# Optimization experiments

Hardware: AMD Instinct MI355X
Metric: run time of the kernel (lower is better)

Reference implementation:

```python
import jax, jax.numpy as jnp
import numpy as np

B, IN_DIM, HID, ATT = 16384, 128, 512, 256
TOTAL = IN_DIM + HID + ATT


def setup_inputs() -> dict:
    key = jax.random.key(0)
    ks = jax.random.split(key, 10)
    u = lambda k, shape, lo, hi: jax.random.uniform(k, shape, jnp.float32, lo, hi)
    return {
        "t": jnp.float32(0.0),
        "h_ltc": jax.random.normal(ks[0], (B, HID), jnp.float32),
        "x_t": jax.random.normal(ks[1], (B, IN_DIM), jnp.float32),
        "context": jax.random.normal(ks[2], (B, ATT), jnp.float32),
        "W_gd": u(ks[3], (2 * HID, TOTAL), -0.1, 0.1),
        "b_gd": u(ks[4], (2 * HID,), -0.1, 0.1),
        "W_tau": u(ks[5], (HID, HID), -0.1, 0.1),
        "b_tau": u(ks[6], (HID,), -0.1, 0.1),
        "gleak": u(ks[7], (HID,), 0.001, 1.0),
        "cm": u(ks[8], (HID,), 0.4, 0.6),
    }


def reference(t, h_ltc, x_t, context, W_gd, b_gd, W_tau, b_tau, gleak, cm):
    # combined: [B, IN+HID+ATT]
    combined = jnp.concatenate([x_t, h_ltc, context], axis=1)
    g_d = combined @ W_gd.T + b_gd            # [B, 2*HID]
    gate, dynamics = jnp.split(g_d, 2, axis=1)
    tau = jax.nn.softplus(h_ltc @ W_tau.T + b_tau)  # [B, HID]
    numerator = jax.nn.sigmoid(gate) * jnp.tanh(dynamics) - h_ltc
    denominator = tau + jax.nn.softplus(cm) + jax.nn.softplus(gleak)
    return numerator / (denominator + 1e-6)
```

## Files before the change

kernel.cpp:

```cpp
#include <hip/hip_runtime.h>
#include <hip/hip_bf16.h>
#include <math.h>

#define BROWS 16384
#define IN_DIM 128
#define HID 512
#define ATT 256
#define KTOT 896
#define KC_TOT 112

typedef __bf16 bf16x8 __attribute__((ext_vector_type(8)));
typedef float f32x4 __attribute__((ext_vector_type(4)));

__device__ __forceinline__ float softplus_f(float x) {
    return fmaxf(x, 0.0f) + log1pf(__expf(-fabsf(x)));
}

__global__ void pack_B(const float* __restrict__ W_gd, const float* __restrict__ W_tau,
                       const float* __restrict__ gleak, const float* __restrict__ cm,
                       __hip_bfloat16* __restrict__ B_stage, float* __restrict__ dconst) {
    const int cid = blockIdx.x * 256 + threadIdx.x;
    if (cid < HID) {
        dconst[cid] = softplus_f(cm[cid]) + softplus_f(gleak[cid]) + 1e-6f;
    }
    const int nl = cid % 192;
    const int kc = (cid / 192) % KC_TOT;
    const int jt = cid / (192 * KC_TOT);
    const int jg = nl / 48, type = (nl % 48) / 16, j16 = nl % 16;
    const int j = jt * 64 + jg * 16 + j16;
    const int k0 = kc * 8;

    float v[8];
    if (type == 0) {
        const float* s = W_gd + (size_t)j * KTOT + k0;
        #pragma unroll
        for (int i = 0; i < 8; ++i) v[i] = s[i];
    } else if (type == 1) {
        const float* s = W_gd + (size_t)(HID + j) * KTOT + k0;
        #pragma unroll
        for (int i = 0; i < 8; ++i) v[i] = s[i];
    } else {
        if (k0 >= IN_DIM && k0 < IN_DIM + HID) {
            const float* s = W_tau + (size_t)j * HID + (k0 - IN_DIM);
            #pragma unroll
            for (int i = 0; i < 8; ++i) v[i] = s[i];
        } else {
            #pragma unroll
            for (int i = 0; i < 8; ++i) v[i] = 0.0f;
        }
    }
    union { __hip_bfloat16 hh[8]; uint4 u; } p;
    #pragma unroll
    for (int i = 0; i < 8; ++i) p.hh[i] = __float2bfloat16(v[i]);
    *(uint4*)(B_stage + (size_t)cid * 8) = p.u;
}

__global__ __launch_bounds__(1024, 4) void ltc_gemm(
    const float* __restrict__ x, const float* __restrict__ h_ltc,
    const float* __restrict__ ctx, const __hip_bfloat16* __restrict__ B_stage,
    const float* __restrict__ b_gd, const float* __restrict__ b_tau,
    const float* __restrict__ dconst, float* __restrict__ out) {

    __shared__ __attribute__((aligned(16))) char As[114688];

    const int mt = blockIdx.x;
    const int tid = threadIdx.x;
    const int wave = tid >> 6, lane = tid & 63;
    const int q = lane >> 4, t = lane & 15;

    const int mi = tid >> 4;
    const int kcg = tid & 15;
    #pragma unroll
    for (int s = 0; s < 7; ++s) {
        const int kc = kcg + 16 * s;
        const float* src; int rs, col;
        if (s == 0)      { src = x;     rs = IN_DIM; col = kcg * 8; }
        else if (s < 5)  { src = h_ltc; rs = HID;    col = kcg * 8 + (s - 1) * 128; }
        else             { src = ctx;   rs = ATT;    col = kcg * 8 + (s - 5) * 128; }
        const float* p = src + (size_t)(mt * 64 + mi) * rs + col;
        float4 v0 = *(const float4*)p;
        float4 v1 = *(const float4*)(p + 4);
        union { __hip_bfloat16 hh[8]; uint4 u; } pk;
        pk.hh[0] = __float2bfloat16(v0.x); pk.hh[1] = __float2bfloat16(v0.y);
        pk.hh[2] = __float2bfloat16(v0.z); pk.hh[3] = __float2bfloat16(v0.w);
        pk.hh[4] = __float2bfloat16(v1.x); pk.hh[5] = __float2bfloat16(v1.y);
        pk.hh[6] = __float2bfloat16(v1.z); pk.hh[7] = __float2bfloat16(v1.w);
        *(uint4*)(As + ((kc * 64 + (mi ^ (kc & 31))) << 4)) = pk.u;
    }
    __syncthreads();

    for (int it = 0; it < 2; ++it) {
        const int jglob = it * 256 + wave * 16;
        const int jt = jglob >> 6;
        const int jg = (jglob >> 4) & 3;
        const __hip_bfloat16* bBase = B_stage
            + ((size_t)jt * (KC_TOT * 192) + jg * 48 + t) * 8;

        f32x4 acc[4][3];
        #pragma unroll
        for (int f = 0; f < 4; ++f)
            #pragma unroll
            for (int ty = 0; ty < 3; ++ty) acc[f][ty] = (f32x4)0.0f;

        bf16x8 ab[2][4]; bf16x8 bb[2][3];

        {
            const int kc = q;
            ab[0][0] = *(const bf16x8*)(As + ((kc * 64 + (t ^ kc)) << 4));
            ab[0][1] = *(const bf16x8*)(As + ((kc * 64 + ((16 + t) ^ kc)) << 4));
            ab[0][2] = *(const bf16x8*)(As + ((kc * 64 + ((32 + t) ^ kc)) << 4));
            ab[0][3] = *(const bf16x8*)(As + ((kc * 64 + ((48 + t) ^ kc)) << 4));
            const __hip_bfloat16* bp = bBase + (size_t)kc * 1536;
            bb[0][0] = *(const bf16x8*)(bp);
            bb[0][1] = *(const bf16x8*)(bp + 128);
        }

        #pragma unroll 4
        for (int kst = 0; kst < 28; ++kst) {
            const int cb = kst & 1, nb = cb ^ 1;
            const bool tau_cur = (kst >= 4 && kst < 20);
            if (kst < 27) {
                const int kc = (kst + 1) * 4 + q;
                const int sw = kc & 31;
                ab[nb][0] = *(const bf16x8*)(As + ((kc * 64 + (t ^ sw)) << 4));
                ab[nb][1] = *(const bf16x8*)(As + ((kc * 64 + ((16 + t) ^ sw)) << 4));
                ab[nb][2] = *(const bf16x8*)(As + ((kc * 64 + ((32 + t) ^ sw)) << 4));
                ab[nb][3] = *(const bf16x8*)(As + ((kc * 64 + ((48 + t) ^ sw)) << 4));
                const __hip_bfloat16* bp = bBase + (size_t)kc * 1536;
                bb[nb][0] = *(const bf16x8*)(bp);
                bb[nb][1] = *(const bf16x8*)(bp + 128);
                if (kst + 1 >= 4 && kst + 1 < 20)
                    bb[nb][2] = *(const bf16x8*)(bp + 256);
            }
            acc[0][0] = __builtin_amdgcn_mfma_f32_16x16x32_bf16(ab[cb][0], bb[cb][0], acc[0][0], 0, 0, 0);
            acc[1][0] = __builtin_amdgcn_mfma_f32_16x16x32_bf16(ab[cb][1], bb[cb][0], acc[1][0], 0, 0, 0);
            acc[2][0] = __builtin_amdgcn_mfma_f32_16x16x32_bf16(ab[cb][2], bb[cb][0], acc[2][0], 0, 0, 0);
            acc[3][0] = __builtin_amdgcn_mfma_f32_16x16x32_bf16(ab[cb][3], bb[cb][0], acc[3][0], 0, 0, 0);
            acc[0][1] = __builtin_amdgcn_mfma_f32_16x16x32_bf16(ab[cb][0], bb[cb][1], acc[0][1], 0, 0, 0);
            acc[1][1] = __builtin_amdgcn_mfma_f32_16x16x32_bf16(ab[cb][1], bb[cb][1], acc[1][1], 0, 0, 0);
            acc[2][1] = __builtin_amdgcn_mfma_f32_16x16x32_bf16(ab[cb][2], bb[cb][1], acc[2][1], 0, 0, 0);
            acc[3][1] = __builtin_amdgcn_mfma_f32_16x16x32_bf16(ab[cb][3], bb[cb][1], acc[3][1], 0, 0, 0);
            if (tau_cur) {
                acc[0][2] = __builtin_amdgcn_mfma_f32_16x16x32_bf16(ab[cb][0], bb[cb][2], acc[0][2], 0, 0, 0);
                acc[1][2] = __builtin_amdgcn_mfma_f32_16x16x32_bf16(ab[cb][1], bb[cb][2], acc[1][2], 0, 0, 0);
                acc[2][2] = __builtin_amdgcn_mfma_f32_16x16x32_bf16(ab[cb][2], bb[cb][2], acc[2][2], 0, 0, 0);
                acc[3][2] = __builtin_amdgcn_mfma_f32_16x16x32_bf16(ab[cb][3], bb[cb][2], acc[3][2], 0, 0, 0);
            }
        }

        const int j = jglob + t;
        const float bgj = b_gd[j];
        const float bdj = b_gd[HID + j];
        const float btj = b_tau[j];
        const float dcj = dconst[j];
        #pragma unroll
        for (int f = 0; f < 4; ++f) {
            #pragma unroll
            for (int r = 0; r < 4; ++r) {
                const int row = mt * 64 + f * 16 + q * 4 + r;
                const float gv = acc[f][0][r] + bgj;
                const float dv = acc[f][1][r] + bdj;
                const float tp = acc[f][2][r] + btj;
                const float hv = h_ltc[(size_t)row * HID + j];
                const float sig = __builtin_amdgcn_rcpf(1.0f + __expf(-gv));
                const float th  = 1.0f - 2.0f * __builtin_amdgcn_rcpf(__expf(2.0f * dv) + 1.0f);
                const float tau = fmaxf(tp, 0.0f) + __logf(1.0f + __expf(-fabsf(tp)));
                out[(size_t)row * HID + j] = (sig * th - hv) * __builtin_amdgcn_rcpf(tau + dcj);
            }
        }
    }
}

extern "C" void kernel_launch(void* const* d_in, const int* in_sizes, int n_in,
                              void* d_out, int out_size, void* d_ws, size_t ws_size,
                              hipStream_t stream) {
    const float* h_ltc = (const float*)d_in[1];
    const float* x_t   = (const float*)d_in[2];
    const float* ctx   = (const float*)d_in[3];
    const float* W_gd  = (const float*)d_in[4];
    const float* b_gd  = (const float*)d_in[5];
    const float* W_tau = (const float*)d_in[6];
    const float* b_tau = (const float*)d_in[7];
    const float* gleak = (const float*)d_in[8];
    const float* cm    = (const float*)d_in[9];

    char* ws = (char*)d_ws;
    __hip_bfloat16* B_stage = (__hip_bfloat16*)ws;
    float* dconst = (float*)(ws + 2752512);

    pack_B<<<672, 256, 0, stream>>>(W_gd, W_tau, gleak, cm, B_stage, dconst);
    ltc_gemm<<<256, 1024, 0, stream>>>(x_t, h_ltc, ctx, B_stage, b_gd, b_tau, dconst,
                                       (float*)d_out);
}
```

Measured before the change: 169.2 us.

## Halve block to 8 waves and deepen register prefetch of A/B fragments

The GEMM block shrinks from 1024 to 512 threads, so each wave covers four column iterations instead of two, and the A-tile staging loop loads two row halves per thread. The fragment pipeline grows from double buffering to a four-slot ring: A fragments are prefetched two k-steps ahead and B fragments from global memory three k-steps ahead. The aim is to hide global B load latency behind more MFMA work. The extra fragments raise register pressure, and fewer waves per block reduce latency hiding from parallelism.

```diff
diff --git a/kernel.cpp b/kernel.cpp
--- a/kernel.cpp
+++ b/kernel.cpp
@@ -55,7 +55,7 @@
     *(uint4*)(B_stage + (size_t)cid * 8) = p.u;
 }
 
-__global__ __launch_bounds__(1024, 4) void ltc_gemm(
+__global__ __launch_bounds__(512, 2) void ltc_gemm(
     const float* __restrict__ x, const float* __restrict__ h_ltc,
     const float* __restrict__ ctx, const __hip_bfloat16* __restrict__ B_stage,
     const float* __restrict__ b_gd, const float* __restrict__ b_tau,
@@ -68,29 +68,33 @@
     const int wave = tid >> 6, lane = tid & 63;
     const int q = lane >> 4, t = lane & 15;
 
-    const int mi = tid >> 4;
+    const int mi0 = tid >> 4;
     const int kcg = tid & 15;
     #pragma unroll
-    for (int s = 0; s < 7; ++s) {
-        const int kc = kcg + 16 * s;
-        const float* src; int rs, col;
-        if (s == 0)      { src = x;     rs = IN_DIM; col = kcg * 8; }
-        else if (s < 5)  { src = h_ltc; rs = HID;    col = kcg * 8 + (s - 1) * 128; }
-        else             { src = ctx;   rs = ATT;    col = kcg * 8 + (s - 5) * 128; }
-        const float* p = src + (size_t)(mt * 64 + mi) * rs + col;
-        float4 v0 = *(const float4*)p;
-        float4 v1 = *(const float4*)(p + 4);
-        union { __hip_bfloat16 hh[8]; uint4 u; } pk;
-        pk.hh[0] = __float2bfloat16(v0.x); pk.hh[1] = __float2bfloat16(v0.y);
-        pk.hh[2] = __float2bfloat16(v0.z); pk.hh[3] = __float2bfloat16(v0.w);
-        pk.hh[4] = __float2bfloat16(v1.x); pk.hh[5] = __float2bfloat16(v1.y);
-        pk.hh[6] = __float2bfloat16(v1.z); pk.hh[7] = __float2bfloat16(v1.w);
-        *(uint4*)(As + ((kc * 64 + (mi ^ (kc & 31))) << 4)) = pk.u;
+    for (int h = 0; h < 2; ++h) {
+        const int mi = mi0 + 32 * h;
+        #pragma unroll
+        for (int s = 0; s < 7; ++s) {
+            const int kc = kcg + 16 * s;
+            const float* src; int rs, col;
+            if (s == 0)      { src = x;     rs = IN_DIM; col = kcg * 8; }
+            else if (s < 5)  { src = h_ltc; rs = HID;    col = kcg * 8 + (s - 1) * 128; }
+            else             { src = ctx;   rs = ATT;    col = kcg * 8 + (s - 5) * 128; }
+            const float* p = src + (size_t)(mt * 64 + mi) * rs + col;
+            float4 v0 = *(const float4*)p;
+            float4 v1 = *(const float4*)(p + 4);
+            union { __hip_bfloat16 hh[8]; uint4 u; } pk;
+            pk.hh[0] = __float2bfloat16(v0.x); pk.hh[1] = __float2bfloat16(v0.y);
+            pk.hh[2] = __float2bfloat16(v0.z); pk.hh[3] = __float2bfloat16(v0.w);
+            pk.hh[4] = __float2bfloat16(v1.x); pk.hh[5] = __float2bfloat16(v1.y);
+            pk.hh[6] = __float2bfloat16(v1.z); pk.hh[7] = __float2bfloat16(v1.w);
+            *(uint4*)(As + ((kc * 64 + (mi ^ (kc & 31))) << 4)) = pk.u;
+        }
     }
     __syncthreads();
 
-    for (int it = 0; it < 2; ++it) {
-        const int jglob = it * 256 + wave * 16;
+    for (int it = 0; it < 4; ++it) {
+        const int jglob = it * 128 + wave * 16;
         const int jt = jglob >> 6;
         const int jg = (jglob >> 4) & 3;
         const __hip_bfloat16* bBase = B_stage
@@ -102,49 +106,59 @@
             #pragma unroll
             for (int ty = 0; ty < 3; ++ty) acc[f][ty] = (f32x4)0.0f;
 
-        bf16x8 ab[2][4]; bf16x8 bb[2][3];
-
-        {
-            const int kc = q;
-            ab[0][0] = *(const bf16x8*)(As + ((kc * 64 + (t ^ kc)) << 4));
-            ab[0][1] = *(const bf16x8*)(As + ((kc * 64 + ((16 + t) ^ kc)) << 4));
-            ab[0][2] = *(const bf16x8*)(As + ((kc * 64 + ((32 + t) ^ kc)) << 4));
-            ab[0][3] = *(const bf16x8*)(As + ((kc * 64 + ((48 + t) ^ kc)) << 4));
-            const __hip_bfloat16* bp = bBase + (size_t)kc * 1536;
-            bb[0][0] = *(const bf16x8*)(bp);
-            bb[0][1] = *(const bf16x8*)(bp + 128);
+        bf16x8 ab[4][4]; bf16x8 bb[4][3];
+
+        #pragma unroll
+        for (int p = 0; p < 2; ++p) {
+            const int kc = p * 4 + q;
+            const int sw = kc & 31;
+            ab[p][0] = *(const bf16x8*)(As + ((kc * 64 + (t ^ sw)) << 4));
+            ab[p][1] = *(const bf16x8*)(As + ((kc * 64 + ((16 + t) ^ sw)) << 4));
+            ab[p][2] = *(const bf16x8*)(As + ((kc * 64 + ((32 + t) ^ sw)) << 4));
+            ab[p][3] = *(const bf16x8*)(As + ((kc * 64 + ((48 + t) ^ sw)) << 4));
+        }
+        #pragma unroll
+        for (int p = 0; p < 3; ++p) {
+            const __hip_bfloat16* bp = bBase + (size_t)(p * 4 + q) * 1536;
+            bb[p][0] = *(const bf16x8*)(bp);
+            bb[p][1] = *(const bf16x8*)(bp + 128);
         }
 
         #pragma unroll 4
         for (int kst = 0; kst < 28; ++kst) {
-            const int cb = kst & 1, nb = cb ^ 1;
+            const int ca = kst & 3;
+            if (kst < 26) {
+                const int kc = (kst + 2) * 4 + q;
+                const int sw = kc & 31;
+                const int na = (kst + 2) & 3;
+                ab[na][0] = *(const bf16x8*)(As + ((kc * 64 + (t ^ sw)) << 4));
+                ab[na][1] = *(const bf16x8*)(As + ((kc * 64 + ((16 + t) ^ sw)) << 4));
+                ab[na][2] = *(const bf16x8*)(As + ((kc * 64 + ((32 + t) ^ sw)) << 4));
+                ab[na][3] = *(const bf16x8*)(As + ((kc * 64 + ((48 + t) ^ sw)) << 4));
+            }
+            if (kst < 25) {
+                const int kc = (kst + 3) * 4 + q;
+                const int nbf = (kst + 3) & 3;
+                const __hip_bfloat16* bp = bBase + (size_t)kc * 1536;
+                bb[nbf][0] = *(const bf16x8*)(bp);
+                bb[nbf][1] = *(const bf16x8*)(bp + 128);
+                if (kst + 3 >= 4 && kst + 3 < 20)
+                    bb[nbf][2] = *(const bf16x8*)(bp + 256);
+            }
             const bool tau_cur = (kst >= 4 && kst < 20);
-            if (kst < 27) {
-                const int kc = (kst + 1) * 4 + q;
-                const int sw = kc & 31;
-                ab[nb][0] = *(const bf16x8*)(As + ((kc * 64 + (t ^ sw)) << 4));
-                ab[nb][1] = *(const bf16x8*)(As + ((kc * 64 + ((16 + t) ^ sw)) << 4));
-                ab[nb][2] = *(const bf16x8*)(As + ((kc * 64 + ((32 + t) ^ sw)) << 4));
-                ab[nb][3] = *(const bf16x8*)(As + ((kc * 64 + ((48 + t) ^ sw)) << 4));
-                const __hip_bfloat16* bp = bBase + (size_t)kc * 1536;
-                bb[nb][0] = *(const bf16x8*)(bp);
-                bb[nb][1] = *(const bf16x8*)(bp + 128);
-                if (kst + 1 >= 4 && kst + 1 < 20)
-                    bb[nb][2] = *(const bf16x8*)(bp + 256);
-            }
-            acc[0][0] = __builtin_amdgcn_mfma_f32_16x16x32_bf16(ab[cb][0], bb[cb][0], acc[0][0], 0, 0, 0);
-            acc[1][0] = __builtin_amdgcn_mfma_f32_16x16x32_bf16(ab[cb][1], bb[cb][0], acc[1][0], 0, 0, 0);
-            acc[2][0] = __builtin_amdgcn_mfma_f32_16x16x32_bf16(ab[cb][2], bb[cb][0], acc[2][0], 0, 0, 0);
-            acc[3][0] = __builtin_amdgcn_mfma_f32_16x16x32_bf16(ab[cb][3], bb[cb][0], acc[3][0], 0, 0, 0);
-            acc[0][1] = __builtin_amdgcn_mfma_f32_16x16x32_bf16(ab[cb][0], bb[cb][1], acc[0][1], 0, 0, 0);
-            acc[1][1] = __builtin_amdgcn_mfma_f32_16x16x32_bf16(ab[cb][1], bb[cb][1], acc[1][1], 0, 0, 0);
-            acc[2][1] = __builtin_amdgcn_mfma_f32_16x16x32_bf16(ab[cb][2], bb[cb][1], acc[2][1], 0, 0, 0);
-            acc[3][1] = __builtin_amdgcn_mfma_f32_16x16x32_bf16(ab[cb][3], bb[cb][1], acc[3][1], 0, 0, 0);
+            acc[0][0] = __builtin_amdgcn_mfma_f32_16x16x32_bf16(ab[ca][0], bb[ca][0], acc[0][0], 0, 0, 0);
+            acc[1][0] = __builtin_amdgcn_mfma_f32_16x16x32_bf16(ab[ca][1], bb[ca][0], acc[1][0], 0, 0, 0);
+            acc[2][0] = __builtin_amdgcn_mfma_f32_16x16x32_bf16(ab[ca][2], bb[ca][0], acc[2][0], 0, 0, 0);
+            acc[3][0] = __builtin_amdgcn_mfma_f32_16x16x32_bf16(ab[ca][3], bb[ca][0], acc[3][0], 0, 0, 0);
+            acc[0][1] = __builtin_amdgcn_mfma_f32_16x16x32_bf16(ab[ca][0], bb[ca][1], acc[0][1], 0, 0, 0);
+            acc[1][1] = __builtin_amdgcn_mfma_f32_16x16x32_bf16(ab[ca][1], bb[ca][1], acc[1][1], 0, 0, 0);
+            acc[2][1] = __builtin_amdgcn_mfma_f32_16x16x32_bf16(ab[ca][2], bb[ca][1], acc[2][1], 0, 0, 0);
+            acc[3][1] = __builtin_amdgcn_mfma_f32_16x16x32_bf16(ab[ca][3], bb[ca][1], acc[3][1], 0, 0, 0);
             if (tau_cur) {
-                acc[0][2] = __builtin_amdgcn_mfma_f32_16x16x32_bf16(ab[cb][0], bb[cb][2], acc[0][2], 0, 0, 0);
-                acc[1][2] = __builtin_amdgcn_mfma_f32_16x16x32_bf16(ab[cb][1], bb[cb][2], acc[1][2], 0, 0, 0);
-                acc[2][2] = __builtin_amdgcn_mfma_f32_16x16x32_bf16(ab[cb][2], bb[cb][2], acc[2][2], 0, 0, 0);
-                acc[3][2] = __builtin_amdgcn_mfma_f32_16x16x32_bf16(ab[cb][3], bb[cb][2], acc[3][2], 0, 0, 0);
+                acc[0][2] = __builtin_amdgcn_mfma_f32_16x16x32_bf16(ab[ca][0], bb[ca][2], acc[0][2], 0, 0, 0);
+                acc[1][2] = __builtin_amdgcn_mfma_f32_16x16x32_bf16(ab[ca][1], bb[ca][2], acc[1][2], 0, 0, 0);
+                acc[2][2] = __builtin_amdgcn_mfma_f32_16x16x32_bf16(ab[ca][2], bb[ca][2], acc[2][2], 0, 0, 0);
+                acc[3][2] = __builtin_amdgcn_mfma_f32_16x16x32_bf16(ab[ca][3], bb[ca][2], acc[3][2], 0, 0, 0);
             }
         }
 
@@ -189,6 +203,6 @@
     float* dconst = (float*)(ws + 2752512);
 
     pack_B<<<672, 256, 0, stream>>>(W_gd, W_tau, gleak, cm, B_stage, dconst);
-    ltc_gemm<<<256, 1024, 0, stream>>>(x_t, h_ltc, ctx, B_stage, b_gd, b_tau, dconst,
-                                       (float*)d_out);
-}
+    ltc_gemm<<<256, 512, 0, stream>>>(x_t, h_ltc, ctx, B_stage, b_gd, b_tau, dconst,
+                                      (float*)d_out);
+}
```

After: 163.2 us. -3.6%, faster.

## Halve block to 8 waves, each computing two 16-column tiles for more A reuse

Applied to the files above, without the earlier changes.

The GEMM block drops from 1024 to 512 threads. Each wave now computes 32 output columns (two 16-wide fragments) instead of 16, so every A fragment read from LDS feeds twice as many MFMAs. The A tile loader is doubled to cover all 64 rows with half the threads. This lowers LDS read traffic per MFMA, but it doubles accumulator and B register usage, leaves fewer waves to hide latency, and the launch bounds change may alter occupancy.

```diff
diff --git a/kernel.cpp b/kernel.cpp
--- a/kernel.cpp
+++ b/kernel.cpp
@@ -55,7 +55,7 @@
     *(uint4*)(B_stage + (size_t)cid * 8) = p.u;
 }
 
-__global__ __launch_bounds__(1024, 4) void ltc_gemm(
+__global__ __launch_bounds__(512, 2) void ltc_gemm(
     const float* __restrict__ x, const float* __restrict__ h_ltc,
     const float* __restrict__ ctx, const __hip_bfloat16* __restrict__ B_stage,
     const float* __restrict__ b_gd, const float* __restrict__ b_tau,
@@ -68,57 +68,65 @@
     const int wave = tid >> 6, lane = tid & 63;
     const int q = lane >> 4, t = lane & 15;
 
-    const int mi = tid >> 4;
+    const int mi0 = tid >> 4;
     const int kcg = tid & 15;
     #pragma unroll
-    for (int s = 0; s < 7; ++s) {
-        const int kc = kcg + 16 * s;
-        const float* src; int rs, col;
-        if (s == 0)      { src = x;     rs = IN_DIM; col = kcg * 8; }
-        else if (s < 5)  { src = h_ltc; rs = HID;    col = kcg * 8 + (s - 1) * 128; }
-        else             { src = ctx;   rs = ATT;    col = kcg * 8 + (s - 5) * 128; }
-        const float* p = src + (size_t)(mt * 64 + mi) * rs + col;
-        float4 v0 = *(const float4*)p;
-        float4 v1 = *(const float4*)(p + 4);
-        union { __hip_bfloat16 hh[8]; uint4 u; } pk;
-        pk.hh[0] = __float2bfloat16(v0.x); pk.hh[1] = __float2bfloat16(v0.y);
-        pk.hh[2] = __float2bfloat16(v0.z); pk.hh[3] = __float2bfloat16(v0.w);
-        pk.hh[4] = __float2bfloat16(v1.x); pk.hh[5] = __float2bfloat16(v1.y);
-        pk.hh[6] = __float2bfloat16(v1.z); pk.hh[7] = __float2bfloat16(v1.w);
-        *(uint4*)(As + ((kc * 64 + (mi ^ (kc & 31))) << 4)) = pk.u;
+    for (int h = 0; h < 2; ++h) {
+        const int mi = mi0 + 32 * h;
+        #pragma unroll
+        for (int s = 0; s < 7; ++s) {
+            const int kc = kcg + 16 * s;
+            const float* src; int rs, col;
+            if (s == 0)      { src = x;     rs = IN_DIM; col = kcg * 8; }
+            else if (s < 5)  { src = h_ltc; rs = HID;    col = kcg * 8 + (s - 1) * 128; }
+            else             { src = ctx;   rs = ATT;    col = kcg * 8 + (s - 5) * 128; }
+            const float* p = src + (size_t)(mt * 64 + mi) * rs + col;
+            float4 v0 = *(const float4*)p;
+            float4 v1 = *(const float4*)(p + 4);
+            union { __hip_bfloat16 hh[8]; uint4 u; } pk;
+            pk.hh[0] = __float2bfloat16(v0.x); pk.hh[1] = __float2bfloat16(v0.y);
+            pk.hh[2] = __float2bfloat16(v0.z); pk.hh[3] = __float2bfloat16(v0.w);
+            pk.hh[4] = __float2bfloat16(v1.x); pk.hh[5] = __float2bfloat16(v1.y);
+            pk.hh[6] = __float2bfloat16(v1.z); pk.hh[7] = __float2bfloat16(v1.w);
+            *(uint4*)(As + ((kc * 64 + (mi ^ (kc & 31))) << 4)) = pk.u;
+        }
     }
     __syncthreads();
 
     for (int it = 0; it < 2; ++it) {
-        const int jglob = it * 256 + wave * 16;
+        const int jglob = it * 256 + wave * 32;
         const int jt = jglob >> 6;
         const int jg = (jglob >> 4) & 3;
         const __hip_bfloat16* bBase = B_stage
             + ((size_t)jt * (KC_TOT * 192) + jg * 48 + t) * 8;
 
-        f32x4 acc[4][3];
-        #pragma unroll
-        for (int f = 0; f < 4; ++f)
-            #pragma unroll
-            for (int ty = 0; ty < 3; ++ty) acc[f][ty] = (f32x4)0.0f;
-
-        bf16x8 ab[2][4]; bf16x8 bb[2][3];
+        f32x4 acc[2][4][3];
+        #pragma unroll
+        for (int jf = 0; jf < 2; ++jf)
+            #pragma unroll
+            for (int f = 0; f < 4; ++f)
+                #pragma unroll
+                for (int ty = 0; ty < 3; ++ty) acc[jf][f][ty] = (f32x4)0.0f;
+
+        bf16x8 ab[2][4]; bf16x8 bb[2][6];
 
         {
             const int kc = q;
-            ab[0][0] = *(const bf16x8*)(As + ((kc * 64 + (t ^ kc)) << 4));
-            ab[0][1] = *(const bf16x8*)(As + ((kc * 64 + ((16 + t) ^ kc)) << 4));
-            ab[0][2] = *(const bf16x8*)(As + ((kc * 64 + ((32 + t) ^ kc)) << 4));
-            ab[0][3] = *(const bf16x8*)(As + ((kc * 64 + ((48 + t) ^ kc)) << 4));
+            const int sw = kc & 31;
+            ab[0][0] = *(const bf16x8*)(As + ((kc * 64 + (t ^ sw)) << 4));
+            ab[0][1] = *(const bf16x8*)(As + ((kc * 64 + ((16 + t) ^ sw)) << 4));
+            ab[0][2] = *(const bf16x8*)(As + ((kc * 64 + ((32 + t) ^ sw)) << 4));
+            ab[0][3] = *(const bf16x8*)(As + ((kc * 64 + ((48 + t) ^ sw)) << 4));
             const __hip_bfloat16* bp = bBase + (size_t)kc * 1536;
             bb[0][0] = *(const bf16x8*)(bp);
             bb[0][1] = *(const bf16x8*)(bp + 128);
+            bb[0][2] = *(const bf16x8*)(bp + 384);
+            bb[0][3] = *(const bf16x8*)(bp + 512);
         }
 
         #pragma unroll 4
         for (int kst = 0; kst < 28; ++kst) {
             const int cb = kst & 1, nb = cb ^ 1;
-            const bool tau_cur = (kst >= 4 && kst < 20);
             if (kst < 27) {
                 const int kc = (kst + 1) * 4 + q;
                 const int sw = kc & 31;
@@ -129,43 +137,51 @@
                 const __hip_bfloat16* bp = bBase + (size_t)kc * 1536;
                 bb[nb][0] = *(const bf16x8*)(bp);
                 bb[nb][1] = *(const bf16x8*)(bp + 128);
-                if (kst + 1 >= 4 && kst + 1 < 20)
-                    bb[nb][2] = *(const bf16x8*)(bp + 256);
-            }
-            acc[0][0] = __builtin_amdgcn_mfma_f32_16x16x32_bf16(ab[cb][0], bb[cb][0], acc[0][0], 0, 0, 0);
-            acc[1][0] = __builtin_amdgcn_mfma_f32_16x16x32_bf16(ab[cb][1], bb[cb][0], acc[1][0], 0, 0, 0);
-            acc[2][0] = __builtin_amdgcn_mfma_f32_16x16x32_bf16(ab[cb][2], bb[cb][0], acc[2][0], 0, 0, 0);
-            acc[3][0] = __builtin_amdgcn_mfma_f32_16x16x32_bf16(ab[cb][3], bb[cb][0], acc[3][0], 0, 0, 0);
-            acc[0][1] = __builtin_amdgcn_mfma_f32_16x16x32_bf16(ab[cb][0], bb[cb][1], acc[0][1], 0, 0, 0);
-            acc[1][1] = __builtin_amdgcn_mfma_f32_16x16x32_bf16(ab[cb][1], bb[cb][1], acc[1][1], 0, 0, 0);
-            acc[2][1] = __builtin_amdgcn_mfma_f32_16x16x32_bf16(ab[cb][2], bb[cb][1], acc[2][1], 0, 0, 0);
-            acc[3][1] = __builtin_amdgcn_mfma_f32_16x16x32_bf16(ab[cb][3], bb[cb][1], acc[3][1], 0, 0, 0);
+                bb[nb][2] = *(const bf16x8*)(bp + 384);
+                bb[nb][3] = *(const bf16x8*)(bp + 512);
+                if (kst + 1 >= 4 && kst + 1 < 20) {
+                    bb[nb][4] = *(const bf16x8*)(bp + 256);
+                    bb[nb][5] = *(const bf16x8*)(bp + 640);
+                }
+            }
+            const bool tau_cur = (kst >= 4 && kst < 20);
+            #pragma unroll
+            for (int f = 0; f < 4; ++f) {
+                acc[0][f][0] = __builtin_amdgcn_mfma_f32_16x16x32_bf16(ab[cb][f], bb[cb][0], acc[0][f][0], 0, 0, 0);
+                acc[1][f][0] = __builtin_amdgcn_mfma_f32_16x16x32_bf16(ab[cb][f], bb[cb][2], acc[1][f][0], 0, 0, 0);
+                acc[0][f][1] = __builtin_amdgcn_mfma_f32_16x16x32_bf16(ab[cb][f], bb[cb][1], acc[0][f][1], 0, 0, 0);
+                acc[1][f][1] = __builtin_amdgcn_mfma_f32_16x16x32_bf16(ab[cb][f], bb[cb][3], acc[1][f][1], 0, 0, 0);
+            }
             if (tau_cur) {
-                acc[0][2] = __builtin_amdgcn_mfma_f32_16x16x32_bf16(ab[cb][0], bb[cb][2], acc[0][2], 0, 0, 0);
-                acc[1][2] = __builtin_amdgcn_mfma_f32_16x16x32_bf16(ab[cb][1], bb[cb][2], acc[1][2], 0, 0, 0);
-                acc[2][2] = __builtin_amdgcn_mfma_f32_16x16x32_bf16(ab[cb][2], bb[cb][2], acc[2][2], 0, 0, 0);
-                acc[3][2] = __builtin_amdgcn_mfma_f32_16x16x32_bf16(ab[cb][3], bb[cb][2], acc[3][2], 0, 0, 0);
-            }
-        }
-
-        const int j = jglob + t;
-        const float bgj = b_gd[j];
-        const float bdj = b_gd[HID + j];
-        const float btj = b_tau[j];
-        const float dcj = dconst[j];
-        #pragma unroll
-        for (int f = 0; f < 4; ++f) {
-            #pragma unroll
-            for (int r = 0; r < 4; ++r) {
-                const int row = mt * 64 + f * 16 + q * 4 + r;
-                const float gv = acc[f][0][r] + bgj;
-                const float dv = acc[f][1][r] + bdj;
-                const float tp = acc[f][2][r] + btj;
-                const float hv = h_ltc[(size_t)row * HID + j];
-                const float sig = __builtin_amdgcn_rcpf(1.0f + __expf(-gv));
-                const float th  = 1.0f - 2.0f * __builtin_amdgcn_rcpf(__expf(2.0f * dv) + 1.0f);
-                const float tau = fmaxf(tp, 0.0f) + __logf(1.0f + __expf(-fabsf(tp)));
-                out[(size_t)row * HID + j] = (sig * th - hv) * __builtin_amdgcn_rcpf(tau + dcj);
+                #pragma unroll
+                for (int f = 0; f < 4; ++f) {
+                    acc[0][f][2] = __builtin_amdgcn_mfma_f32_16x16x32_bf16(ab[cb][f], bb[cb][4], acc[0][f][2], 0, 0, 0);
+                    acc[1][f][2] = __builtin_amdgcn_mfma_f32_16x16x32_bf16(ab[cb][f], bb[cb][5], acc[1][f][2], 0, 0, 0);
+                }
+            }
+        }
+
+        #pragma unroll
+        for (int jf = 0; jf < 2; ++jf) {
+            const int j = jglob + jf * 16 + t;
+            const float bgj = b_gd[j];
+            const float bdj = b_gd[HID + j];
+            const float btj = b_tau[j];
+            const float dcj = dconst[j];
+            #pragma unroll
+            for (int f = 0; f < 4; ++f) {
+                #pragma unroll
+                for (int r = 0; r < 4; ++r) {
+                    const int row = mt * 64 + f * 16 + q * 4 + r;
+                    const float gv = acc[jf][f][0][r] + bgj;
+                    const float dv = acc[jf][f][1][r] + bdj;
+                    const float tp = acc[jf][f][2][r] + btj;
+                    const float hv = h_ltc[(size_t)row * HID + j];
+                    const float sig = __builtin_amdgcn_rcpf(1.0f + __expf(-gv));
+                    const float th  = 1.0f - 2.0f * __builtin_amdgcn_rcpf(__expf(2.0f * dv) + 1.0f);
+                    const float tau = fmaxf(tp, 0.0f) + __logf(1.0f + __expf(-fabsf(tp)));
+                    out[(size_t)row * HID + j] = (sig * th - hv) * __builtin_amdgcn_rcpf(tau + dcj);
+                }
             }
         }
     }
@@ -189,6 +205,6 @@
     float* dconst = (float*)(ws + 2752512);
 
     pack_B<<<672, 256, 0, stream>>>(W_gd, W_tau, gleak, cm, B_stage, dconst);
-    ltc_gemm<<<256, 1024, 0, stream>>>(x_t, h_ltc, ctx, B_stage, b_gd, b_tau, dconst,
-                                       (float*)d_out);
-}
+    ltc_gemm<<<256, 512, 0, stream>>>(x_t, h_ltc, ctx, B_stage, b_gd, b_tau, dconst,
+                                      (float*)d_out);
+}
```

After: 161.7 us. 4.5% less time.
